# Performance work log

Measured on AMD Instinct MI355X. Metric: run time of the kernel, lower is better.

Reference implementation:

```python
import jax, jax.numpy as jnp
import numpy as np

MEM_SIZE = 100000
EMB = 1024
HEADS = 8
HEAD_DIM = EMB // HEADS
TOPK = 10
BATCH = 2048


def setup_inputs() -> dict:
    key = jax.random.key(0)
    ks = jax.random.split(key, 10)
    query = jax.random.normal(ks[0], (BATCH, EMB), dtype=jnp.float32)
    memory = jax.random.normal(ks[1], (MEM_SIZE, EMB), dtype=jnp.float32) * 0.1
    s = 1.0 / np.sqrt(EMB)
    w_q = jax.random.normal(ks[2], (EMB, EMB), dtype=jnp.float32) * s
    w_k = jax.random.normal(ks[3], (EMB, EMB), dtype=jnp.float32) * s
    w_v = jax.random.normal(ks[4], (EMB, EMB), dtype=jnp.float32) * s
    b_q = jnp.zeros((EMB,), jnp.float32)
    b_k = jnp.zeros((EMB,), jnp.float32)
    b_v = jnp.zeros((EMB,), jnp.float32)
    w_o = jax.random.normal(ks[5], (EMB, EMB), dtype=jnp.float32) * s
    b_o = jnp.zeros((EMB,), jnp.float32)
    return {"query": query, "memory": memory, "w_q": w_q, "w_k": w_k,
            "w_v": w_v, "b_q": b_q, "b_k": b_k, "b_v": b_v,
            "w_o": w_o, "b_o": b_o}


def reference(query, memory, w_q, w_k, w_v, b_q, b_k, b_v, w_o, b_o):
    B = query.shape[0]
    # similarity + top-k retrieval: [B, M] -> indices [B, K]
    sim = jnp.matmul(query, memory.T)
    _, idx = jax.lax.top_k(sim, TOPK)
    mem_sel = memory[idx]                       # [B, K, E] gather
    # MultiheadAttention: query is one token, keys/values = retrieved memories
    q = (query @ w_q.T + b_q).reshape(B, HEADS, HEAD_DIM)
    k = (mem_sel @ w_k.T + b_k).reshape(B, TOPK, HEADS, HEAD_DIM)
    v = (mem_sel @ w_v.T + b_v).reshape(B, TOPK, HEADS, HEAD_DIM)
    scale = 1.0 / np.sqrt(HEAD_DIM)
    scores = jnp.einsum('bhd,bkhd->bhk', q, k) * scale   # [B, H, K]
    attn = jax.nn.softmax(scores, axis=-1)
    ctx = jnp.einsum('bhk,bkhd->bhd', attn, v).reshape(B, EMB)
    return ctx @ w_o.T + b_o
```

## Files before the change

kernel.cpp:

```cpp
#include <hip/hip_runtime.h>
#include <cstdint>
#include <cstddef>

#define BATCH   2048
#define EMB     1024
#define HEADS   8
#define HDIM    128
#define TOPK    10
#define MEMN    100000
#define NTILES  782
#define CHUNKS  64
#define TPC     13
#define CAND    20
#define SCALE   0.08838834764831845f


typedef _Float16 h16;
typedef _Float16 half8 __attribute__((ext_vector_type(8)));
typedef _Float16 half4 __attribute__((ext_vector_type(4)));
typedef float    f32x4 __attribute__((ext_vector_type(4)));

__device__ __forceinline__ void gl_lds16(const void* g, void* l) {
  __builtin_amdgcn_global_load_lds(
      (const __attribute__((address_space(1))) unsigned int*)g,
      (__attribute__((address_space(3))) unsigned int*)l, 16, 0, 0);
}

__device__ __forceinline__ void bar_sync() {
  asm volatile("" ::: "memory");
  __builtin_amdgcn_s_barrier();
  __builtin_amdgcn_sched_barrier(0);
}
__device__ __forceinline__ void bar_wait6() {
  asm volatile("s_waitcnt vmcnt(6)" ::: "memory");
  __builtin_amdgcn_s_barrier();
  __builtin_amdgcn_sched_barrier(0);
}
__device__ __forceinline__ void bar_wait0() {
  asm volatile("s_waitcnt vmcnt(0)" ::: "memory");
  __builtin_amdgcn_s_barrier();
  __builtin_amdgcn_sched_barrier(0);
}

template <int N>
__device__ __forceinline__ void topk_ins(float (&tv)[N], int (&ti)[N],
                                         float s, int gi) {
  float cv = s; int ci = gi;
#pragma unroll
  for (int j = 0; j < N; ++j) {
    bool sw = tv[j] < cv;
    float tf = tv[j]; int tt = ti[j];
    if (sw) { tv[j] = cv; ti[j] = ci; cv = tf; ci = tt; }
  }
}

__global__ void __launch_bounds__(256) k_f2h(
    const float* __restrict__ in, h16* __restrict__ out, long n4)
{
  long i = (long)blockIdx.x * 256 + threadIdx.x;
  const long stride = (long)gridDim.x * 256;
  for (; i < n4; i += stride) {
    const f32x4 v = ((const f32x4*)in)[i];
    half4 o;
#pragma unroll
    for (int j = 0; j < 4; ++j) o[j] = (h16)v[j];
    ((half4*)out)[i] = o;
  }
}

__global__ void __launch_bounds__(256) k_f2h3(
    const float* __restrict__ a, const float* __restrict__ b,
    const float* __restrict__ c,
    h16* __restrict__ oa, h16* __restrict__ ob, h16* __restrict__ oc)
{
  const float* in = (blockIdx.y == 0) ? a : (blockIdx.y == 1) ? b : c;
  h16* out       = (blockIdx.y == 0) ? oa : (blockIdx.y == 1) ? ob : oc;
  const long i = (long)blockIdx.x * 256 + threadIdx.x;
  const f32x4 v = ((const f32x4*)in)[i];
  half4 o;
#pragma unroll
  for (int j = 0; j < 4; ++j) o[j] = (h16)v[j];
  ((half4*)out)[i] = o;
}

__global__ void __launch_bounds__(256) k_f2hT(
    const float* __restrict__ in, h16* __restrict__ out)
{
  __shared__ float tl[64][65];
  const int n0 = blockIdx.x * 64, e0 = blockIdx.y * 64;
  const int cc = threadIdx.x & 63, rb = threadIdx.x >> 6;
#pragma unroll
  for (int i = 0; i < 16; ++i) {
    const int r = i * 4 + rb;
    tl[r][cc] = in[(size_t)(n0 + r) * EMB + e0 + cc];
  }
  __syncthreads();
#pragma unroll
  for (int i = 0; i < 16; ++i) {
    const int r = i * 4 + rb;
    out[(size_t)(e0 + r) * EMB + n0 + cc] = (h16)tl[cc][r];
  }
}

__device__ __forceinline__ void sim_stage2(
    const h16* __restrict__ query, const h16* __restrict__ memory,
    char* smem, int buf, int r0, int n0, int k0, int w, int l)
{
  h16* dA = (h16*)(smem + buf * 32768);
  h16* dB = (h16*)(smem + 65536 + buf * 16384);
#pragma unroll
  for (int i = 0; i < 4; ++i) {
    const int ch = i * 512 + w * 64 + l;
    const int row = ch >> 3;
    const int kc = (ch & 7) ^ (row & 7);
    gl_lds16(query + (size_t)(r0 + row) * EMB + k0 + kc * 8,
             dA + (size_t)(i * 512 + w * 64) * 8);
  }
#pragma unroll
  for (int i = 0; i < 2; ++i) {
    const int ch = i * 512 + w * 64 + l;
    const int row = ch >> 3;
    const int kc = (ch & 7) ^ (row & 7);
    int n = n0 + row; if (n > MEMN - 1) n = MEMN - 1;
    gl_lds16(memory + (size_t)n * EMB + k0 + kc * 8,
             dB + (size_t)(i * 512 + w * 64) * 8);
  }
}

__device__ __forceinline__ void sim_comp2(
    const char* smem, int buf, int wr, int wc, int l, f32x4 (&acc)[4][4])
{
  const h16* sA = (const h16*)(smem + buf * 32768);
  const h16* sB = (const h16*)(smem + 65536 + buf * 16384);
#pragma unroll
  for (int ks = 0; ks < 2; ++ks) {
    half8 af[4], bfr[4];
#pragma unroll
    for (int mi = 0; mi < 4; ++mi) {
      const int row = wr * 64 + mi * 16 + (l & 15);
      const int slot = (ks * 4 + (l >> 4)) ^ (row & 7);
      af[mi] = *(const half8*)&sA[row * 64 + slot * 8];
    }
#pragma unroll
    for (int ni = 0; ni < 4; ++ni) {
      const int row = wc * 64 + ni * 16 + (l & 15);
      const int slot = (ks * 4 + (l >> 4)) ^ (row & 7);
      bfr[ni] = *(const half8*)&sB[row * 64 + slot * 8];
    }
    __builtin_amdgcn_s_setprio(1);
#pragma unroll
    for (int mi = 0; mi < 4; ++mi)
#pragma unroll
      for (int ni = 0; ni < 4; ++ni)
        acc[mi][ni] = __builtin_amdgcn_mfma_f32_16x16x32_f16(
            af[mi], bfr[ni], acc[mi][ni], 0, 0, 0);
    __builtin_amdgcn_s_setprio(0);
  }
}

__global__ void __launch_bounds__(512) k_sim_h(
    const h16* __restrict__ query, const h16* __restrict__ memory,
    float* __restrict__ cand_val, int* __restrict__ cand_idx)
{
  const int c  = blockIdx.y;
  const int r0 = blockIdx.x * 256;
  __shared__ __align__(16) char smem[98304];
  float* lS = (float*)smem;

  const int t = threadIdx.x, w = t >> 6, l = t & 63;
  const int wr = w >> 1, wc = w & 1;
  const int row_s = t >> 2, qq = t & 3;

  float tvA[TOPK], tvB[TOPK]; int tiA[TOPK], tiB[TOPK];
#pragma unroll
  for (int j = 0; j < TOPK; ++j) { tvA[j] = -3.0e38f; tvB[j] = -3.0e38f; tiA[j] = 0; tiB[j] = 0; }

  const int tile_beg = c * TPC;
  int tile_end = tile_beg + TPC; if (tile_end > NTILES) tile_end = NTILES;

  for (int tile = tile_beg; tile < tile_end; ++tile) {
    const int n0 = tile * 128;
    f32x4 acc[4][4] = {};

    sim_stage2(query, memory, smem, 0, r0, n0, 0, w, l);
#pragma unroll 1
    for (int kt = 0; kt < 14; kt += 2) {
      sim_stage2(query, memory, smem, 1, r0, n0, (kt + 1) * 64, w, l);
      bar_wait6();
      sim_comp2(smem, 0, wr, wc, l, acc);
      bar_sync();
      sim_stage2(query, memory, smem, 0, r0, n0, (kt + 2) * 64, w, l);
      bar_wait6();
      sim_comp2(smem, 1, wr, wc, l, acc);
      bar_sync();
    }
    sim_stage2(query, memory, smem, 1, r0, n0, 15 * 64, w, l);
    bar_wait6();
    sim_comp2(smem, 0, wr, wc, l, acc);
    bar_sync();
    bar_wait0();
    sim_comp2(smem, 1, wr, wc, l, acc);
    __syncthreads();

#pragma unroll
    for (int ph = 0; ph < 2; ++ph) {
      if ((wr >> 1) == ph) {
#pragma unroll
        for (int mi = 0; mi < 4; ++mi)
#pragma unroll
          for (int ni = 0; ni < 4; ++ni)
#pragma unroll
            for (int r = 0; r < 4; ++r) {
              const int row_l = (wr & 1) * 64 + mi * 16 + (l >> 4) * 4 + r;
              const int col = wc * 64 + ni * 16 + (l & 15);
              lS[row_l * 132 + col] = acc[mi][ni][r];
            }
      }
      __syncthreads();
      float (&tv)[TOPK] = ph ? tvB : tvA; int (&ti)[TOPK] = ph ? tiB : tiA;
#pragma unroll
      for (int cc = 0; cc < 8; ++cc) {
        const int c4 = qq * 32 + ((cc + qq * 2) & 7) * 4;
        const f32x4 v = *(const f32x4*)&lS[row_s * 132 + c4];
        const float m = fmaxf(fmaxf(v[0], v[1]), fmaxf(v[2], v[3]));
        if (m > tv[TOPK - 1]) {
#pragma unroll
          for (int j = 0; j < 4; ++j) {
            const int g = n0 + c4 + j;
            if (g < MEMN && v[j] > tv[TOPK - 1]) topk_ins<TOPK>(tv, ti, v[j], g);
          }
        }
      }
      __syncthreads();
    }
  }

  float* lSv = (float*)smem;
  int*   lSi = (int*)(smem + 20480);
#pragma unroll
  for (int ph = 0; ph < 2; ++ph) {
#pragma unroll
    for (int j = 0; j < TOPK; ++j) {
      lSv[row_s * 40 + qq * TOPK + j] = ph ? tvB[j] : tvA[j];
      lSi[row_s * 40 + qq * TOPK + j] = ph ? tiB[j] : tiA[j];
    }
    __syncthreads();
    if (qq == 0) {
      float fv[TOPK]; int fi[TOPK];
#pragma unroll
      for (int j = 0; j < TOPK; ++j) { fv[j] = -3.0e38f; fi[j] = 0; }
      for (int m = 0; m < 40; ++m) {
        const float s = lSv[row_s * 40 + m];
        if (s > fv[TOPK - 1]) topk_ins<TOPK>(fv, fi, s, lSi[row_s * 40 + m]);
      }
      const int grow = r0 + ph * 128 + row_s;
#pragma unroll
      for (int j = 0; j < TOPK; ++j) {
        cand_val[(size_t)(c * TOPK + j) * BATCH + grow] = fv[j];
        cand_idx[(size_t)(c * TOPK + j) * BATCH + grow] = fi[j];
      }
    }
    __syncthreads();
  }
}

__global__ void __launch_bounds__(256) k_sim_f32(
    const float* __restrict__ query, const float* __restrict__ memory,
    float* __restrict__ cand_val, int* __restrict__ cand_idx)
{
  const int c  = blockIdx.x;
  const int r0 = blockIdx.y * 128;
  __shared__ __align__(16) char smem[65536];
  float* lA = (float*)smem;
  float* lB = (float*)(smem + 32768);
  float* lS = (float*)smem;

  const int t = threadIdx.x, w = t >> 6, l = t & 63;
  const int wr = w >> 1, wc = w & 1;
  const int row_s = t >> 2, qq = t & 3;

  float tvA[TOPK], tvB[TOPK]; int tiA[TOPK], tiB[TOPK];
#pragma unroll
  for (int j = 0; j < TOPK; ++j) { tvA[j] = -3.0e38f; tvB[j] = -3.0e38f; tiA[j] = 0; tiB[j] = 0; }

  const int tile_beg = c * TPC;
  int tile_end = tile_beg + TPC; if (tile_end > NTILES) tile_end = NTILES;

  for (int tile = tile_beg; tile < tile_end; ++tile) {
    const int n0 = tile * 128;
    f32x4 acc[4][4] = {};

    for (int kt = 0; kt < 16; ++kt) {
      const int k0 = kt * 64;
#pragma unroll
      for (int i = 0; i < 8; ++i) {
        const int c16 = (w * 8 + i) * 64 + l;
        const int row = c16 >> 4, s16 = c16 & 15;
        const int src = s16 ^ (row & 7);
        gl_lds16(query + (size_t)(r0 + row) * EMB + k0 + src * 4,
                 lA + (size_t)(w * 8 + i) * 256);
        int n = n0 + row; if (n > MEMN - 1) n = MEMN - 1;
        gl_lds16(memory + (size_t)n * EMB + k0 + src * 4,
                 lB + (size_t)(w * 8 + i) * 256);
      }
      __syncthreads();
#pragma unroll
      for (int ks = 0; ks < 2; ++ks) {
        half8 af[4], bfr[4];
#pragma unroll
        for (int mi = 0; mi < 4; ++mi) {
          const int row = wr * 64 + mi * 16 + (l & 15);
          const int g = ks * 4 + (l >> 4), m7 = row & 7;
          const f32x4 a0 = *(const f32x4*)(lA + row * 64 + (((2 * g)     ^ m7) << 2));
          const f32x4 a1 = *(const f32x4*)(lA + row * 64 + (((2 * g + 1) ^ m7) << 2));
          half8 f;
#pragma unroll
          for (int j = 0; j < 4; ++j) { f[j] = (h16)a0[j]; f[4 + j] = (h16)a1[j]; }
          af[mi] = f;
        }
#pragma unroll
        for (int ni = 0; ni < 4; ++ni) {
          const int row = wc * 64 + ni * 16 + (l & 15);
          const int g = ks * 4 + (l >> 4), m7 = row & 7;
          const f32x4 b0 = *(const f32x4*)(lB + row * 64 + (((2 * g)     ^ m7) << 2));
          const f32x4 b1 = *(const f32x4*)(lB + row * 64 + (((2 * g + 1) ^ m7) << 2));
          half8 f;
#pragma unroll
          for (int j = 0; j < 4; ++j) { f[j] = (h16)b0[j]; f[4 + j] = (h16)b1[j]; }
          bfr[ni] = f;
        }
#pragma unroll
        for (int mi = 0; mi < 4; ++mi)
#pragma unroll
          for (int ni = 0; ni < 4; ++ni)
            acc[mi][ni] = __builtin_amdgcn_mfma_f32_16x16x32_f16(
                af[mi], bfr[ni], acc[mi][ni], 0, 0, 0);
      }
      __syncthreads();
    }

#pragma unroll
    for (int ph = 0; ph < 2; ++ph) {
      if (wr == ph) {
#pragma unroll
        for (int mi = 0; mi < 4; ++mi)
#pragma unroll
          for (int ni = 0; ni < 4; ++ni)
#pragma unroll
            for (int r = 0; r < 4; ++r) {
              const int row_l = mi * 16 + (l >> 4) * 4 + r;
              const int col = wc * 64 + ni * 16 + (l & 15);
              lS[row_l * 131 + col] = acc[mi][ni][r];
            }
      }
      __syncthreads();
      float (&tv)[TOPK] = ph ? tvB : tvA; int (&ti)[TOPK] = ph ? tiB : tiA;
#pragma unroll 8
      for (int cc = 0; cc < 32; ++cc) {
        const int colt = qq * 32 + ((cc + qq * 8) & 31);
        const float s = lS[row_s * 131 + colt];
        const int g = n0 + colt;
        if (g < MEMN && s > tv[TOPK - 1]) topk_ins<TOPK>(tv, ti, s, g);
      }
      __syncthreads();
    }
  }

  float* lSv = (float*)smem;
  int*   lSi = (int*)(smem + 10240);
#pragma unroll
  for (int ph = 0; ph < 2; ++ph) {
#pragma unroll
    for (int j = 0; j < TOPK; ++j) {
      lSv[row_s * 40 + qq * TOPK + j] = ph ? tvB[j] : tvA[j];
      lSi[row_s * 40 + qq * TOPK + j] = ph ? tiB[j] : tiA[j];
    }
    __syncthreads();
    if (qq == 0) {
      float fv[TOPK]; int fi[TOPK];
#pragma unroll
      for (int j = 0; j < TOPK; ++j) { fv[j] = -3.0e38f; fi[j] = 0; }
      for (int m = 0; m < 40; ++m) {
        const float s = lSv[row_s * 40 + m];
        if (s > fv[TOPK - 1]) topk_ins<TOPK>(fv, fi, s, lSi[row_s * 40 + m]);
      }
      const int grow = r0 + ph * 64 + row_s;
#pragma unroll
      for (int j = 0; j < TOPK; ++j) {
        cand_val[(size_t)(c * TOPK + j) * BATCH + grow] = fv[j];
        cand_idx[(size_t)(c * TOPK + j) * BATCH + grow] = fi[j];
      }
    }
    __syncthreads();
  }
}

__global__ void __launch_bounds__(256) k_merge20(
    const float* __restrict__ cand_val, const int* __restrict__ cand_idx,
    int* __restrict__ idx20, int nch)
{
  const int row = blockIdx.x * 256 + threadIdx.x;
  float tv[CAND]; int ti[CAND];
#pragma unroll
  for (int j = 0; j < CAND; ++j) { tv[j] = -3.0e38f; ti[j] = 0; }
  for (int m = 0; m < nch * TOPK; ++m) {
    const float s = cand_val[(size_t)m * BATCH + row];
    if (s > tv[CAND - 1]) {
      const int gi = cand_idx[(size_t)m * BATCH + row];
      topk_ins<CAND>(tv, ti, s, gi);
    }
  }
#pragma unroll
  for (int j = 0; j < CAND; ++j) idx20[row * CAND + j] = ti[j];
}

__global__ void __launch_bounds__(256) k_rescore(
    const float* __restrict__ query, const float* __restrict__ memory,
    const int* __restrict__ idx20, int* __restrict__ idx10)
{
  const int w = threadIdx.x >> 6, l = threadIdx.x & 63;
  const int b = blockIdx.x * 4 + w;
  const float* qp = query + (size_t)b * EMB + l * 16;
  float q[16];
#pragma unroll
  for (int j = 0; j < 4; ++j) {
    const f32x4 v = *(const f32x4*)(qp + 4 * j);
#pragma unroll
    for (int i = 0; i < 4; ++i) q[j * 4 + i] = v[i];
  }
  double sc[CAND];
#pragma unroll
  for (int cc = 0; cc < CAND; ++cc) {
    const int mi = idx20[b * CAND + cc];
    const float* mp = memory + (size_t)mi * EMB + l * 16;
    double s = 0.0;
#pragma unroll
    for (int j = 0; j < 4; ++j) {
      const f32x4 v = *(const f32x4*)(mp + 4 * j);
#pragma unroll
      for (int i = 0; i < 4; ++i) s += (double)q[j * 4 + i] * (double)v[i];
    }
#pragma unroll
    for (int o = 1; o < 64; o <<= 1) s += __shfl_xor(s, o);
    sc[cc] = s;
  }
  if (l == 0) {
    unsigned used = 0;
#pragma unroll
    for (int j = 0; j < TOPK; ++j) {
      double best = -1.0e300; int bi = 0;
#pragma unroll
      for (int cc = 0; cc < CAND; ++cc)
        if (!((used >> cc) & 1u) && sc[cc] > best) { best = sc[cc]; bi = cc; }
      used |= 1u << bi;
      idx10[b * TOPK + j] = idx20[b * CAND + bi];
    }
  }
}

__global__ void __launch_bounds__(256) k_gemm16(
    const h16* __restrict__ A, int astr, int acol, int aoffz,
    const h16* __restrict__ Bt, int bcol, int boffz,
    const float* __restrict__ bias, int biasoffz,
    h16* __restrict__ outH, float* __restrict__ outF,
    int cstr, int ccol, int coffz, int nkt)
{
  const int z = blockIdx.z;
  acol += z * aoffz; bcol += z * boffz; ccol += z * coffz;
  const float* bp = bias ? bias + z * biasoffz : nullptr;

  const int c0 = blockIdx.x * 128, r0 = blockIdx.y * 128;
  __shared__ __align__(16) h16 lA[128 * 64], lB[128 * 64];
  const int t = threadIdx.x, w = t >> 6, l = t & 63;
  const int wr = w >> 1, wc = w & 1;
  f32x4 acc[4][4] = {};

  for (int kt = 0; kt < nkt; ++kt) {
    const int k0 = kt * 64;
#pragma unroll
    for (int i = 0; i < 4; ++i) {
      const int ch = w * 256 + i * 64 + l;
      const int row = ch >> 3;
      const int kc = (ch & 7) ^ (row & 7);
      gl_lds16(A  + (size_t)(r0 + row) * astr + acol + k0 + kc * 8,
               lA + (size_t)(w * 256 + i * 64) * 8);
      gl_lds16(Bt + (size_t)(c0 + row) * EMB + bcol + k0 + kc * 8,
               lB + (size_t)(w * 256 + i * 64) * 8);
    }
    __syncthreads();
#pragma unroll
    for (int ks = 0; ks < 2; ++ks) {
      half8 af[4], bfr[4];
#pragma unroll
      for (int mi = 0; mi < 4; ++mi) {
        const int row = wr * 64 + mi * 16 + (l & 15);
        const int slot = (ks * 4 + (l >> 4)) ^ (row & 7);
        af[mi] = *(const half8*)&lA[row * 64 + slot * 8];
      }
#pragma unroll
      for (int ni = 0; ni < 4; ++ni) {
        const int row = wc * 64 + ni * 16 + (l & 15);
        const int slot = (ks * 4 + (l >> 4)) ^ (row & 7);
        bfr[ni] = *(const half8*)&lB[row * 64 + slot * 8];
      }
#pragma unroll
      for (int mi = 0; mi < 4; ++mi)
#pragma unroll
        for (int ni = 0; ni < 4; ++ni)
          acc[mi][ni] = __builtin_amdgcn_mfma_f32_16x16x32_f16(
              af[mi], bfr[ni], acc[mi][ni], 0, 0, 0);
    }
    __syncthreads();
  }
#pragma unroll
  for (int ni = 0; ni < 4; ++ni) {
    const int ncol = c0 + wc * 64 + ni * 16 + (l & 15);
    const float bv = bp ? bp[ncol] : 0.0f;
#pragma unroll
    for (int mi = 0; mi < 4; ++mi)
#pragma unroll
      for (int r = 0; r < 4; ++r) {
        const int grow = r0 + wr * 64 + mi * 16 + (l >> 4) * 4 + r;
        const float v = acc[mi][ni][r] + bv;
        if (outH) outH[(size_t)grow * cstr + ccol + ncol] = (h16)v;
        else      outF[(size_t)grow * cstr + ccol + ncol] = v;
      }
  }
}

__global__ void __launch_bounds__(256) k_attn(
    const float* __restrict__ memory, const int* __restrict__ idx10,
    h16* __restrict__ qtA)
{
  const int w = threadIdx.x >> 6, l = threadIdx.x & 63;
  const int b = blockIdx.x * 4 + w;
  int rows[TOPK];
#pragma unroll
  for (int k = 0; k < TOPK; ++k) rows[k] = idx10[b * TOPK + k];

  for (int h = 0; h < HEADS; ++h) {
    h16* qp = qtA + (size_t)b * (HEADS * EMB) + h * EMB + l * 16;
    const half8 qa = *(const half8*)qp;
    const half8 qb = *(const half8*)(qp + 8);
    float qf[16];
#pragma unroll
    for (int j = 0; j < 8; ++j) { qf[j] = (float)qa[j]; qf[8 + j] = (float)qb[j]; }

    float mrun = -3.0e38f, den = 0.f;
    float acc[16];
#pragma unroll
    for (int j = 0; j < 16; ++j) acc[j] = 0.f;

#pragma unroll
    for (int k = 0; k < TOPK; ++k) {
      const float* mp = memory + (size_t)rows[k] * EMB + l * 16;
      float mv[16]; float p = 0.f;
#pragma unroll
      for (int j = 0; j < 4; ++j) {
        const f32x4 m = *(const f32x4*)(mp + 4 * j);
#pragma unroll
        for (int i = 0; i < 4; ++i) { mv[j * 4 + i] = m[i]; p += qf[j * 4 + i] * m[i]; }
      }
#pragma unroll
      for (int o = 1; o < 64; o <<= 1) p += __shfl_xor(p, o);
      p *= SCALE;
      if (p > mrun) {
        const float rs = __expf(mrun - p);
        den *= rs;
#pragma unroll
        for (int j = 0; j < 16; ++j) acc[j] *= rs;
        mrun = p;
      }
      const float e = __expf(p - mrun);
      den += e;
#pragma unroll
      for (int j = 0; j < 16; ++j) acc[j] += e * mv[j];
    }
    const float inv = 1.0f / den;
    half8 o0, o1;
#pragma unroll
    for (int j = 0; j < 8; ++j) {
      o0[j] = (h16)(acc[j] * inv);
      o1[j] = (h16)(acc[8 + j] * inv);
    }
    *(half8*)qp = o0;
    *(half8*)(qp + 8) = o1;
  }
}

extern "C" void kernel_launch(void* const* d_in, const int* in_sizes, int n_in,
                              void* d_out, int out_size, void* d_ws, size_t ws_size,
                              hipStream_t stream)
{
  const float* query  = (const float*)d_in[0];
  const float* memory = (const float*)d_in[1];
  const float* w_q    = (const float*)d_in[2];
  const float* w_k    = (const float*)d_in[3];
  const float* w_v    = (const float*)d_in[4];
  const float* b_q    = (const float*)d_in[5];
  const float* b_v    = (const float*)d_in[7];
  const float* w_o    = (const float*)d_in[8];
  const float* b_o    = (const float*)d_in[9];

  char* ws = (char*)d_ws;
  float* cand_val = (float*)(ws + 0);
  int*   cand_idx = (int*)  (ws + 5242880);
  int*   idx20    = (int*)  (ws + 10485760);
  int*   idx10    = (int*)  (ws + 10649600);
  h16*   qH       = (h16*)  (ws + 10731520);
  h16*   wqH      = (h16*)  (ws + 14925824);
  h16*   wkTH     = (h16*)  (ws + 17022976);
  h16*   wvH      = (h16*)  (ws + 19120128);
  h16*   woH      = (h16*)  (ws + 21217280);
  h16*   qpH      = (h16*)  (ws + 23314432);
  h16*   qtA      = (h16*)  (ws + 27508736);
  h16*   ctxH     = (h16*)  (ws + 61063168);
  h16*   memH     = (h16*)  (ws + 65257472);

  const bool fast = ws_size >= 270057472ULL;

  if (fast) k_f2h<<<8192, 256, 0, stream>>>(memory, memH, 25600000L);
  k_f2h <<<2048, 256, 0, stream>>>(query, qH, 524288L);
  k_f2h3<<<dim3(1024, 3), 256, 0, stream>>>(w_q, w_v, w_o, wqH, wvH, woH);
  k_f2hT<<<dim3(16, 16), 256, 0, stream>>>(w_k, wkTH);

  if (fast) k_sim_h  <<<dim3(8, CHUNKS), 512, 0, stream>>>(qH, memH, cand_val, cand_idx);
  else      k_sim_f32<<<dim3(CHUNKS, 16), 256, 0, stream>>>(query, memory, cand_val, cand_idx);
  k_merge20<<<BATCH / 256, 256, 0, stream>>>(cand_val, cand_idx, idx20, CHUNKS);
  k_rescore<<<BATCH / 4, 256, 0, stream>>>(query, memory, idx20, idx10);

  k_gemm16<<<dim3(8, 16), 256, 0, stream>>>(qH, EMB, 0, 0, wqH, 0, 0,
                                            b_q, 0, qpH, nullptr, EMB, 0, 0, 16);
  k_gemm16<<<dim3(8, 16, 8), 256, 0, stream>>>(qpH, EMB, 0, HDIM, wkTH, 0, HDIM,
                                               nullptr, 0, qtA, nullptr,
                                               HEADS * EMB, 0, EMB, 2);
  k_attn<<<BATCH / 4, 256, 0, stream>>>(memory, idx10, qtA);
  k_gemm16<<<dim3(1, 16, 8), 256, 0, stream>>>(qtA, HEADS * EMB, 0, EMB,
                                               wvH, 0, HDIM * EMB,
                                               b_v, HDIM, ctxH, nullptr,
                                               EMB, 0, HDIM, 16);
  k_gemm16<<<dim3(8, 16), 256, 0, stream>>>(ctxH, EMB, 0, 0, woH, 0, 0,
                                            b_o, 0, nullptr, (float*)d_out,
                                            EMB, 0, 0, 16);
}
```

Measured before the change: 2.549 ms.

## Halve K-tile depth and LDS footprint, restructure top-k scan to one list per thread

The similarity GEMM now stages 32-wide K slices instead of 64-wide, cutting shared memory from 96KB to 48KB so more blocks can be resident per CU. The number of pipeline steps doubles, along with barriers, and the vmcnt wait is adjusted to match. The per-tile top-k scan now gives each thread a single 10-entry list over half a row, scanned in four row phases, instead of two lists over quarter rows. This lowers register pressure and the final merge work. The cost is more synchronization per tile and more serialized scan phases.

```diff
diff --git a/kernel.cpp b/kernel.cpp
--- a/kernel.cpp
+++ b/kernel.cpp
@@ -31,8 +31,8 @@
   __builtin_amdgcn_s_barrier();
   __builtin_amdgcn_sched_barrier(0);
 }
-__device__ __forceinline__ void bar_wait6() {
-  asm volatile("s_waitcnt vmcnt(6)" ::: "memory");
+__device__ __forceinline__ void bar_wait3() {
+  asm volatile("s_waitcnt vmcnt(3)" ::: "memory");
   __builtin_amdgcn_s_barrier();
   __builtin_amdgcn_sched_barrier(0);
 }
@@ -106,56 +106,52 @@
     const h16* __restrict__ query, const h16* __restrict__ memory,
     char* smem, int buf, int r0, int n0, int k0, int w, int l)
 {
-  h16* dA = (h16*)(smem + buf * 32768);
-  h16* dB = (h16*)(smem + 65536 + buf * 16384);
-#pragma unroll
-  for (int i = 0; i < 4; ++i) {
+  h16* dA = (h16*)(smem + buf * 16384);
+  h16* dB = (h16*)(smem + 32768 + buf * 8192);
+#pragma unroll
+  for (int i = 0; i < 2; ++i) {
     const int ch = i * 512 + w * 64 + l;
-    const int row = ch >> 3;
-    const int kc = (ch & 7) ^ (row & 7);
+    const int row = ch >> 2;
+    const int kc = (ch & 3) ^ (row & 3);
     gl_lds16(query + (size_t)(r0 + row) * EMB + k0 + kc * 8,
              dA + (size_t)(i * 512 + w * 64) * 8);
   }
-#pragma unroll
-  for (int i = 0; i < 2; ++i) {
-    const int ch = i * 512 + w * 64 + l;
-    const int row = ch >> 3;
-    const int kc = (ch & 7) ^ (row & 7);
+  {
+    const int ch = w * 64 + l;
+    const int row = ch >> 2;
+    const int kc = (ch & 3) ^ (row & 3);
     int n = n0 + row; if (n > MEMN - 1) n = MEMN - 1;
     gl_lds16(memory + (size_t)n * EMB + k0 + kc * 8,
-             dB + (size_t)(i * 512 + w * 64) * 8);
+             dB + (size_t)(w * 64) * 8);
   }
 }
 
 __device__ __forceinline__ void sim_comp2(
     const char* smem, int buf, int wr, int wc, int l, f32x4 (&acc)[4][4])
 {
-  const h16* sA = (const h16*)(smem + buf * 32768);
-  const h16* sB = (const h16*)(smem + 65536 + buf * 16384);
-#pragma unroll
-  for (int ks = 0; ks < 2; ++ks) {
-    half8 af[4], bfr[4];
-#pragma unroll
-    for (int mi = 0; mi < 4; ++mi) {
-      const int row = wr * 64 + mi * 16 + (l & 15);
-      const int slot = (ks * 4 + (l >> 4)) ^ (row & 7);
-      af[mi] = *(const half8*)&sA[row * 64 + slot * 8];
-    }
-#pragma unroll
-    for (int ni = 0; ni < 4; ++ni) {
-      const int row = wc * 64 + ni * 16 + (l & 15);
-      const int slot = (ks * 4 + (l >> 4)) ^ (row & 7);
-      bfr[ni] = *(const half8*)&sB[row * 64 + slot * 8];
-    }
-    __builtin_amdgcn_s_setprio(1);
-#pragma unroll
-    for (int mi = 0; mi < 4; ++mi)
-#pragma unroll
-      for (int ni = 0; ni < 4; ++ni)
-        acc[mi][ni] = __builtin_amdgcn_mfma_f32_16x16x32_f16(
-            af[mi], bfr[ni], acc[mi][ni], 0, 0, 0);
-    __builtin_amdgcn_s_setprio(0);
-  }
+  const h16* sA = (const h16*)(smem + buf * 16384);
+  const h16* sB = (const h16*)(smem + 32768 + buf * 8192);
+  half8 af[4], bfr[4];
+#pragma unroll
+  for (int mi = 0; mi < 4; ++mi) {
+    const int row = wr * 64 + mi * 16 + (l & 15);
+    const int slot = (l >> 4) ^ (row & 3);
+    af[mi] = *(const half8*)&sA[row * 32 + slot * 8];
+  }
+#pragma unroll
+  for (int ni = 0; ni < 4; ++ni) {
+    const int row = wc * 64 + ni * 16 + (l & 15);
+    const int slot = (l >> 4) ^ (row & 3);
+    bfr[ni] = *(const half8*)&sB[row * 32 + slot * 8];
+  }
+  __builtin_amdgcn_s_setprio(1);
+#pragma unroll
+  for (int mi = 0; mi < 4; ++mi)
+#pragma unroll
+    for (int ni = 0; ni < 4; ++ni)
+      acc[mi][ni] = __builtin_amdgcn_mfma_f32_16x16x32_f16(
+          af[mi], bfr[ni], acc[mi][ni], 0, 0, 0);
+  __builtin_amdgcn_s_setprio(0);
 }
 
 __global__ void __launch_bounds__(512) k_sim_h(
@@ -164,16 +160,16 @@
 {
   const int c  = blockIdx.y;
   const int r0 = blockIdx.x * 256;
-  __shared__ __align__(16) char smem[98304];
+  __shared__ __align__(16) char smem[49152];
   float* lS = (float*)smem;
 
   const int t = threadIdx.x, w = t >> 6, l = t & 63;
   const int wr = w >> 1, wc = w & 1;
-  const int row_s = t >> 2, qq = t & 3;
-
-  float tvA[TOPK], tvB[TOPK]; int tiA[TOPK], tiB[TOPK];
-#pragma unroll
-  for (int j = 0; j < TOPK; ++j) { tvA[j] = -3.0e38f; tvB[j] = -3.0e38f; tiA[j] = 0; tiB[j] = 0; }
+  const int row_s = t >> 1, qq = t & 1;
+
+  float tv[TOPK]; int ti[TOPK];
+#pragma unroll
+  for (int j = 0; j < TOPK; ++j) { tv[j] = -3.0e38f; ti[j] = 0; }
 
   const int tile_beg = c * TPC;
   int tile_end = tile_beg + TPC; if (tile_end > NTILES) tile_end = NTILES;
@@ -184,18 +180,18 @@
 
     sim_stage2(query, memory, smem, 0, r0, n0, 0, w, l);
 #pragma unroll 1
-    for (int kt = 0; kt < 14; kt += 2) {
-      sim_stage2(query, memory, smem, 1, r0, n0, (kt + 1) * 64, w, l);
-      bar_wait6();
+    for (int kt = 0; kt < 30; kt += 2) {
+      sim_stage2(query, memory, smem, 1, r0, n0, (kt + 1) * 32, w, l);
+      bar_wait3();
       sim_comp2(smem, 0, wr, wc, l, acc);
       bar_sync();
-      sim_stage2(query, memory, smem, 0, r0, n0, (kt + 2) * 64, w, l);
-      bar_wait6();
+      sim_stage2(query, memory, smem, 0, r0, n0, (kt + 2) * 32, w, l);
+      bar_wait3();
       sim_comp2(smem, 1, wr, wc, l, acc);
       bar_sync();
     }
-    sim_stage2(query, memory, smem, 1, r0, n0, 15 * 64, w, l);
-    bar_wait6();
+    sim_stage2(query, memory, smem, 1, r0, n0, 31 * 32, w, l);
+    bar_wait3();
     sim_comp2(smem, 0, wr, wc, l, acc);
     bar_sync();
     bar_wait0();
@@ -203,31 +199,35 @@
     __syncthreads();
 
 #pragma unroll
-    for (int ph = 0; ph < 2; ++ph) {
-      if ((wr >> 1) == ph) {
+    for (int p = 0; p < 4; ++p) {
+      if (wr == p) {
 #pragma unroll
         for (int mi = 0; mi < 4; ++mi)
 #pragma unroll
           for (int ni = 0; ni < 4; ++ni)
 #pragma unroll
             for (int r = 0; r < 4; ++r) {
-              const int row_l = (wr & 1) * 64 + mi * 16 + (l >> 4) * 4 + r;
+              const int rl = mi * 16 + (l >> 4) * 4 + r;
               const int col = wc * 64 + ni * 16 + (l & 15);
-              lS[row_l * 132 + col] = acc[mi][ni][r];
+              lS[rl * 132 + col] = acc[mi][ni][r];
             }
       }
       __syncthreads();
-      float (&tv)[TOPK] = ph ? tvB : tvA; int (&ti)[TOPK] = ph ? tiB : tiA;
-#pragma unroll
-      for (int cc = 0; cc < 8; ++cc) {
-        const int c4 = qq * 32 + ((cc + qq * 2) & 7) * 4;
-        const f32x4 v = *(const f32x4*)&lS[row_s * 132 + c4];
-        const float m = fmaxf(fmaxf(v[0], v[1]), fmaxf(v[2], v[3]));
-        if (m > tv[TOPK - 1]) {
-#pragma unroll
-          for (int j = 0; j < 4; ++j) {
-            const int g = n0 + c4 + j;
-            if (g < MEMN && v[j] > tv[TOPK - 1]) topk_ins<TOPK>(tv, ti, v[j], g);
+      if ((row_s >> 6) == p) {
+        const int rl = row_s & 63;
+#pragma unroll
+        for (int cc = 0; cc < 16; ++cc) {
+          const int i4 = (cc + ((rl & 15))) & 15;
+          const int colb = qq * 64 + i4 * 4;
+          const f32x4 v = *(const f32x4*)&lS[rl * 132 + colb];
+          const float m = fmaxf(fmaxf(v[0], v[1]), fmaxf(v[2], v[3]));
+          if (m > tv[TOPK - 1]) {
+#pragma unroll
+            for (int j = 0; j < 4; ++j) {
+              const int g = n0 + colb + j;
+              if (g < MEMN && v[j] > tv[TOPK - 1])
+                topk_ins<TOPK>(tv, ti, v[j], g);
+            }
           }
         }
       }
@@ -238,29 +238,25 @@
   float* lSv = (float*)smem;
   int*   lSi = (int*)(smem + 20480);
 #pragma unroll
-  for (int ph = 0; ph < 2; ++ph) {
+  for (int j = 0; j < TOPK; ++j) {
+    lSv[row_s * 20 + qq * TOPK + j] = tv[j];
+    lSi[row_s * 20 + qq * TOPK + j] = ti[j];
+  }
+  __syncthreads();
+  if (qq == 0) {
+    float fv[TOPK]; int fi[TOPK];
+#pragma unroll
+    for (int j = 0; j < TOPK; ++j) { fv[j] = -3.0e38f; fi[j] = 0; }
+    for (int m = 0; m < 20; ++m) {
+      const float s = lSv[row_s * 20 + m];
+      if (s > fv[TOPK - 1]) topk_ins<TOPK>(fv, fi, s, lSi[row_s * 20 + m]);
+    }
+    const int grow = r0 + row_s;
 #pragma unroll
     for (int j = 0; j < TOPK; ++j) {
-      lSv[row_s * 40 + qq * TOPK + j] = ph ? tvB[j] : tvA[j];
-      lSi[row_s * 40 + qq * TOPK + j] = ph ? tiB[j] : tiA[j];
-    }
-    __syncthreads();
-    if (qq == 0) {
-      float fv[TOPK]; int fi[TOPK];
-#pragma unroll
-      for (int j = 0; j < TOPK; ++j) { fv[j] = -3.0e38f; fi[j] = 0; }
-      for (int m = 0; m < 40; ++m) {
-        const float s = lSv[row_s * 40 + m];
-        if (s > fv[TOPK - 1]) topk_ins<TOPK>(fv, fi, s, lSi[row_s * 40 + m]);
-      }
-      const int grow = r0 + ph * 128 + row_s;
-#pragma unroll
-      for (int j = 0; j < TOPK; ++j) {
-        cand_val[(size_t)(c * TOPK + j) * BATCH + grow] = fv[j];
-        cand_idx[(size_t)(c * TOPK + j) * BATCH + grow] = fi[j];
-      }
-    }
-    __syncthreads();
+      cand_val[(size_t)(c * TOPK + j) * BATCH + grow] = fv[j];
+      cand_idx[(size_t)(c * TOPK + j) * BATCH + grow] = fi[j];
+    }
   }
 }
 
```

Result: slower. 5.076 ms (+99.1%).

## Split top-20 merge across four threads per row and batch conversion kernels

Applied to the files above, without the earlier changes.

The top-20 merge kernel now uses four threads per batch row, each scanning a quarter of the 640 chunk candidates. The four partial lists are then combined in shared memory by one thread. This raises parallelism from 8 blocks to 32 blocks, at the cost of a second merge pass. The memory fp32-to-fp16 conversion now handles 8 elements per thread, and the query and weight conversions are fused into one launch to cut launch overhead.

```diff
diff --git a/kernel.cpp b/kernel.cpp
--- a/kernel.cpp
+++ b/kernel.cpp
@@ -54,33 +54,38 @@
   }
 }
 
-__global__ void __launch_bounds__(256) k_f2h(
-    const float* __restrict__ in, h16* __restrict__ out, long n4)
+__global__ void __launch_bounds__(256) k_f2hW(
+    const float* __restrict__ in, h16* __restrict__ out, long n8)
 {
   long i = (long)blockIdx.x * 256 + threadIdx.x;
   const long stride = (long)gridDim.x * 256;
-  for (; i < n4; i += stride) {
-    const f32x4 v = ((const f32x4*)in)[i];
-    half4 o;
-#pragma unroll
-    for (int j = 0; j < 4; ++j) o[j] = (h16)v[j];
-    ((half4*)out)[i] = o;
-  }
-}
-
-__global__ void __launch_bounds__(256) k_f2h3(
-    const float* __restrict__ a, const float* __restrict__ b,
-    const float* __restrict__ c,
-    h16* __restrict__ oa, h16* __restrict__ ob, h16* __restrict__ oc)
-{
-  const float* in = (blockIdx.y == 0) ? a : (blockIdx.y == 1) ? b : c;
-  h16* out       = (blockIdx.y == 0) ? oa : (blockIdx.y == 1) ? ob : oc;
+  for (; i < n8; i += stride) {
+    const f32x4 a = ((const f32x4*)in)[2 * i];
+    const f32x4 b = ((const f32x4*)in)[2 * i + 1];
+    half8 o;
+#pragma unroll
+    for (int j = 0; j < 4; ++j) { o[j] = (h16)a[j]; o[4 + j] = (h16)b[j]; }
+    ((half8*)out)[i] = o;
+  }
+}
+
+__global__ void __launch_bounds__(256) k_convA(
+    const float* __restrict__ q,  const float* __restrict__ wq,
+    const float* __restrict__ wv, const float* __restrict__ wo,
+    h16* __restrict__ qH, h16* __restrict__ wqH,
+    h16* __restrict__ wvH, h16* __restrict__ woH)
+{
   const long i = (long)blockIdx.x * 256 + threadIdx.x;
-  const f32x4 v = ((const f32x4*)in)[i];
+  const float* in; h16* out; long off;
+  if (i < 524288)        { in = q;  out = qH;  off = i; }
+  else if (i < 786432)   { in = wq; out = wqH; off = i - 524288; }
+  else if (i < 1048576)  { in = wv; out = wvH; off = i - 786432; }
+  else                   { in = wo; out = woH; off = i - 1048576; }
+  const f32x4 v = ((const f32x4*)in)[off];
   half4 o;
 #pragma unroll
   for (int j = 0; j < 4; ++j) o[j] = (h16)v[j];
-  ((half4*)out)[i] = o;
+  ((half4*)out)[off] = o;
 }
 
 __global__ void __launch_bounds__(256) k_f2hT(
@@ -397,13 +402,18 @@
 
 __global__ void __launch_bounds__(256) k_merge20(
     const float* __restrict__ cand_val, const int* __restrict__ cand_idx,
-    int* __restrict__ idx20, int nch)
-{
-  const int row = blockIdx.x * 256 + threadIdx.x;
+    int* __restrict__ idx20)
+{
+  __shared__ float lv[64 * 80];
+  __shared__ int   li[64 * 80];
+  const int rl = threadIdx.x >> 2, qq = threadIdx.x & 3;
+  const int row = blockIdx.x * 64 + rl;
+
   float tv[CAND]; int ti[CAND];
 #pragma unroll
   for (int j = 0; j < CAND; ++j) { tv[j] = -3.0e38f; ti[j] = 0; }
-  for (int m = 0; m < nch * TOPK; ++m) {
+  const int m0 = qq * 160;
+  for (int m = m0; m < m0 + 160; ++m) {
     const float s = cand_val[(size_t)m * BATCH + row];
     if (s > tv[CAND - 1]) {
       const int gi = cand_idx[(size_t)m * BATCH + row];
@@ -411,7 +421,22 @@
     }
   }
 #pragma unroll
-  for (int j = 0; j < CAND; ++j) idx20[row * CAND + j] = ti[j];
+  for (int j = 0; j < CAND; ++j) {
+    lv[rl * 80 + qq * CAND + j] = tv[j];
+    li[rl * 80 + qq * CAND + j] = ti[j];
+  }
+  __syncthreads();
+  if (qq == 0) {
+    float fv[CAND]; int fi[CAND];
+#pragma unroll
+    for (int j = 0; j < CAND; ++j) { fv[j] = -3.0e38f; fi[j] = 0; }
+    for (int m = 0; m < 80; ++m) {
+      const float s = lv[rl * 80 + m];
+      if (s > fv[CAND - 1]) topk_ins<CAND>(fv, fi, s, li[rl * 80 + m]);
+    }
+#pragma unroll
+    for (int j = 0; j < CAND; ++j) idx20[row * CAND + j] = fi[j];
+  }
 }
 
 __global__ void __launch_bounds__(256) k_rescore(
@@ -619,14 +644,13 @@
 
   const bool fast = ws_size >= 270057472ULL;
 
-  if (fast) k_f2h<<<8192, 256, 0, stream>>>(memory, memH, 25600000L);
-  k_f2h <<<2048, 256, 0, stream>>>(query, qH, 524288L);
-  k_f2h3<<<dim3(1024, 3), 256, 0, stream>>>(w_q, w_v, w_o, wqH, wvH, woH);
+  if (fast) k_f2hW<<<8192, 256, 0, stream>>>(memory, memH, 12800000L);
+  k_convA<<<5120, 256, 0, stream>>>(query, w_q, w_v, w_o, qH, wqH, wvH, woH);
   k_f2hT<<<dim3(16, 16), 256, 0, stream>>>(w_k, wkTH);
 
   if (fast) k_sim_h  <<<dim3(8, CHUNKS), 512, 0, stream>>>(qH, memH, cand_val, cand_idx);
   else      k_sim_f32<<<dim3(CHUNKS, 16), 256, 0, stream>>>(query, memory, cand_val, cand_idx);
-  k_merge20<<<BATCH / 256, 256, 0, stream>>>(cand_val, cand_idx, idx20, CHUNKS);
+  k_merge20<<<BATCH / 64, 256, 0, stream>>>(cand_val, cand_idx, idx20);
   k_rescore<<<BATCH / 4, 256, 0, stream>>>(query, memory, idx20, idx10);
 
   k_gemm16<<<dim3(8, 16), 256, 0, stream>>>(qH, EMB, 0, 0, wqH, 0, 0,
```

Result: faster. 2.161 ms (-15.2%).
